# Optimization experiments

Hardware: AMD Instinct MI355X
Metric: run time of the kernel (lower is better)

## Reference

```python
import jax, jax.numpy as jnp
import numpy as np

B, T, D, E, H, F, K = 4, 2048, 2048, 16, 1024, 1024, 2


def setup_inputs() -> dict:
    key = jax.random.key(0)
    ks = jax.random.split(key, 7)
    sD, sH, sF = D ** -0.5, H ** -0.5, F ** -0.5
    hidden_state = jax.random.normal(ks[0], (B, T, D), jnp.float32)
    Wr = jax.random.normal(ks[1], (D, E), jnp.float32) * sD      # router
    Wg = jax.random.normal(ks[2], (D, 1), jnp.float32) * sD      # shared gate
    W1 = jax.random.normal(ks[3], (E, D, H), jnp.float32) * sD   # expert up-proj
    W2 = jax.random.normal(ks[4], (E, H, D), jnp.float32) * sH   # expert down-proj
    W1s = jax.random.normal(ks[5], (D, F), jnp.float32) * sD     # shared expert up
    W2s = jax.random.normal(ks[6], (F, D), jnp.float32) * sF     # shared expert down
    return {"hidden_state": hidden_state, "Wr": Wr, "Wg": Wg,
            "W1": W1, "W2": W2, "W1s": W1s, "W2s": W2s}


def reference(hidden_state, Wr, Wg, W1, W2, W1s, W2s):
    b, t, d = hidden_state.shape
    N = b * t
    x = hidden_state.reshape(N, d)

    # Router: softmax scores + shared-expert sigmoid gate
    s = jax.nn.softmax(x @ Wr, axis=-1)           # [N, E]
    g_shared = jax.nn.sigmoid(x @ Wg)             # [N, 1]

    topk_vals, topk_idx = jax.lax.top_k(s, K)     # [N, K]

    # Dense combine weights: gate[n,e] = topk_vals if expert e chosen, else 0.
    # Mathematically identical to sort/gather/scatter-add dispatch in the source.
    gate = jnp.zeros((N, E), dtype=s.dtype).at[
        jnp.arange(N)[:, None], topk_idx].add(topk_vals)

    # Per-expert FFN (fixed small expert loop), gate-weighted combine
    y = jnp.zeros_like(x)
    for e in range(E):
        h = jax.nn.gelu(x @ W1[e], approximate=False)   # [N, H]
        y = y + gate[:, e:e + 1] * (h @ W2[e])

    # Shared expert, scaled by sigmoid gate
    shared = jax.nn.gelu(x @ W1s, approximate=False) @ W2s
    y = y + g_shared * shared
    y_out = y.reshape(b, t, d)

    # Aux stats (attention_mask is None branch)
    importance = s.mean(axis=0)                               # [E]
    counts = jnp.zeros((E,), jnp.float32).at[topk_idx.reshape(-1)].add(1.0)
    load = counts / (counts.sum() + 1e-12)
    return y_out, importance, load
```

## Files before the change

### kernel.cpp

```cpp
#include <hip/hip_runtime.h>
#include <hip/hip_bf16.h>


#define N_TOK 8192
#define DDIM  2048
#define NEXP  16
#define HDIM  1024
#define FDIM  1024
#define NASSIGN (N_TOK * 2)

typedef __attribute__((ext_vector_type(8))) short bf16x8;
typedef __attribute__((ext_vector_type(4))) float f32x4;
typedef __attribute__((ext_vector_type(8))) unsigned short u16x8;
typedef __attribute__((ext_vector_type(4))) unsigned short u16x4;

__device__ inline unsigned short f2bf(float f) {
    unsigned int u = __builtin_bit_cast(unsigned int, f);
    u += 0x7FFFu + ((u >> 16) & 1u);
    return (unsigned short)(u >> 16);
}

__device__ inline float gelu_f(float v) {
    return 0.5f * v * (1.0f + erff(v * 0.7071067811865475f));
}

__device__ inline void gld16(void* lds, const void* g) {
    __builtin_amdgcn_global_load_lds(
        (const __attribute__((address_space(1))) unsigned int*)g,
        (__attribute__((address_space(3))) unsigned int*)lds, 16, 0, 0);
}

__global__ __launch_bounds__(256) void zero_small(float* imp) {
    if (threadIdx.x < NEXP) imp[threadIdx.x] = 0.0f;
}

__global__ __launch_bounds__(256) void cast_x_kernel(const float* __restrict__ x,
                                                     unsigned short* __restrict__ xb) {
    size_t i = (size_t)blockIdx.x * 256 + threadIdx.x;
    const float4 a = ((const float4*)x)[i * 2];
    const float4 b = ((const float4*)x)[i * 2 + 1];
    u16x8 o;
    o[0] = f2bf(a.x); o[1] = f2bf(a.y); o[2] = f2bf(a.z); o[3] = f2bf(a.w);
    o[4] = f2bf(b.x); o[5] = f2bf(b.y); o[6] = f2bf(b.z); o[7] = f2bf(b.w);
    *(u16x8*)(xb + i * 8) = o;
}

template <int R, int C>
__global__ __launch_bounds__(256) void transpose_cast(const float* __restrict__ src,
                                                      unsigned short* __restrict__ dst) {
    __shared__ unsigned short t[64][66];
    const size_t zoff = (size_t)blockIdx.z * R * C;
    src += zoff; dst += zoff;
    const int r0 = blockIdx.y * 64, c0 = blockIdx.x * 64;
    const int tid = threadIdx.x;
    const int cr = tid >> 4;
    const int cc4 = (tid & 15) * 4;
#pragma unroll
    for (int it = 0; it < 4; ++it) {
        int row = cr + it * 16;
        const float4 v = *(const float4*)(src + (size_t)(r0 + row) * C + c0 + cc4);
        t[row][cc4 + 0] = f2bf(v.x); t[row][cc4 + 1] = f2bf(v.y);
        t[row][cc4 + 2] = f2bf(v.z); t[row][cc4 + 3] = f2bf(v.w);
    }
    __syncthreads();
#pragma unroll
    for (int it = 0; it < 4; ++it) {
        int cc = cr + it * 16;
        u16x4 o;
#pragma unroll
        for (int j = 0; j < 4; ++j) o[j] = t[cc4 + j][cc];
        *(u16x4*)(dst + (size_t)(c0 + cc) * R + r0 + cc4) = o;
    }
}

__global__ __launch_bounds__(256) void router_kernel(
    const float* __restrict__ x, const float* __restrict__ Wr, const float* __restrict__ Wg,
    float* __restrict__ gsh, int* __restrict__ t2i, float* __restrict__ t2v,
    float* __restrict__ imp) {
    __shared__ float simp[NEXP];
    const int tid = threadIdx.x, lane = tid & 63, w = tid >> 6;
    if (tid < NEXP) simp[tid] = 0.0f;
    __syncthreads();
    const int n = blockIdx.x * 4 + w;
    const float* xr = x + (size_t)n * DDIM;
    float acc[NEXP];
#pragma unroll
    for (int e = 0; e < NEXP; ++e) acc[e] = 0.0f;
    float ag = 0.0f;
    for (int j = 0; j < DDIM / 64; ++j) {
        int d = lane + j * 64;
        float xv = xr[d];
        const float* wr = Wr + (size_t)d * NEXP;
#pragma unroll
        for (int e = 0; e < NEXP; ++e) acc[e] = fmaf(xv, wr[e], acc[e]);
        ag = fmaf(xv, Wg[d], ag);
    }
#pragma unroll
    for (int off = 32; off; off >>= 1) {
#pragma unroll
        for (int e = 0; e < NEXP; ++e) acc[e] += __shfl_xor(acc[e], off);
        ag += __shfl_xor(ag, off);
    }
    if (lane == 0) {
        float mx = acc[0];
#pragma unroll
        for (int e = 1; e < NEXP; ++e) mx = fmaxf(mx, acc[e]);
        float p[NEXP], s = 0.0f;
#pragma unroll
        for (int e = 0; e < NEXP; ++e) { p[e] = expf(acc[e] - mx); s += p[e]; }
        const float inv = 1.0f / s;
        int i1 = 0; float v1 = -1.0f;
#pragma unroll
        for (int e = 0; e < NEXP; ++e) {
            p[e] *= inv;
            if (p[e] > v1) { v1 = p[e]; i1 = e; }
        }
        int i2 = 0; float v2 = -1.0f;
#pragma unroll
        for (int e = 0; e < NEXP; ++e) {
            if (e != i1 && p[e] > v2) { v2 = p[e]; i2 = e; }
        }
        t2i[2 * n] = i1; t2i[2 * n + 1] = i2;
        t2v[2 * n] = v1; t2v[2 * n + 1] = v2;
        gsh[n] = 1.0f / (1.0f + expf(-ag));
#pragma unroll
        for (int e = 0; e < NEXP; ++e) atomicAdd(&simp[e], p[e]);
    }
    __syncthreads();
    if (tid < NEXP) unsafeAtomicAdd(&imp[tid], simp[tid]);
}

__global__ __launch_bounds__(256) void scan_finalize(
    const int* __restrict__ t2i, const float* __restrict__ imp,
    int* __restrict__ offs, int* __restrict__ fill, float* __restrict__ out_tail) {
    __shared__ int hist[NEXP];
    const int tid = threadIdx.x;
    if (tid < NEXP) hist[tid] = 0;
    __syncthreads();
    for (int i = tid; i < NASSIGN; i += 256) atomicAdd(&hist[t2i[i]], 1);
    __syncthreads();
    if (tid == 0) {
        int o = 0;
        for (int e = 0; e < NEXP; ++e) { offs[e] = o; o += hist[e]; }
        offs[NEXP] = o;
    }
    if (tid < NEXP) {
        fill[tid] = 0;
        out_tail[tid] = imp[tid] * (1.0f / (float)N_TOK);
        out_tail[NEXP + tid] = (float)hist[tid] / (float)NASSIGN;
    }
}

__global__ __launch_bounds__(256) void build_assign(
    const int* __restrict__ t2i, const float* __restrict__ t2v,
    const int* __restrict__ offs, int* __restrict__ fill,
    int* __restrict__ atok, float* __restrict__ agate) {
    const int n = blockIdx.x * 256 + threadIdx.x;
#pragma unroll
    for (int k = 0; k < 2; ++k) {
        int e = t2i[2 * n + k];
        int pos = offs[e] + atomicAdd(&fill[e], 1);
        atok[pos] = n;
        agate[pos] = t2v[2 * n + k];
    }
}

template <int MODE>
__global__ __launch_bounds__(256) void gemm_tile(
    const unsigned short* __restrict__ A, const unsigned short* __restrict__ B,
    float* __restrict__ Y, unsigned short* __restrict__ Hb,
    const int* __restrict__ offs, const int* __restrict__ atok,
    const float* __restrict__ agate, const float* __restrict__ gsh) {
    constexpr int KD = (MODE == 0 || MODE == 2) ? DDIM : HDIM;
    constexpr int NC = (MODE == 0 || MODE == 2) ? HDIM : DDIM;
    const int e = blockIdx.z;
    int m0 = 0, mE = N_TOK;
    if (MODE <= 1) { m0 = offs[e]; mE = offs[e + 1] - m0; }
    const int tm = blockIdx.y;
    if (tm * 128 >= mE) return;
    const int n0 = blockIdx.x * 128;

    __shared__ __align__(16) unsigned short As[128 * 32];
    __shared__ __align__(16) unsigned short Bs[128 * 32];

    const int tid = threadIdx.x, lane = tid & 63;
    const int wid = tid >> 6, wm = wid >> 1, wn = wid & 1;

    const unsigned short* srcA[2];
    const unsigned short* srcB[2];
    char* dstA[2];
    char* dstB[2];
#pragma unroll
    for (int it = 0; it < 2; ++it) {
        int c = tid + it * 256;
        int row = c >> 2, slot = c & 3;
        int ksw = (slot ^ ((row >> 1) & 3)) * 8;
        int arow = tm * 128 + row;
        if (MODE == 0) {
            int ar = arow < mE ? arow : mE - 1;
            srcA[it] = A + (size_t)atok[m0 + ar] * DDIM + ksw;
        } else if (MODE == 1) {
            int ar = arow < mE ? arow : mE - 1;
            srcA[it] = A + (size_t)(m0 + ar) * HDIM + ksw;
        } else {
            srcA[it] = A + (size_t)arow * KD + ksw;
        }
        srcB[it] = B + (MODE <= 1 ? (size_t)e * KD * NC : (size_t)0)
                     + (size_t)(n0 + row) * KD + ksw;
        dstA[it] = (char*)As + c * 16;
        dstB[it] = (char*)Bs + c * 16;
    }

    f32x4 acc[4][4] = {};

#pragma unroll 1
    for (int kk = 0; kk < KD; kk += 32) {
        if (kk) __syncthreads();
        gld16(dstA[0], srcA[0] + kk);
        gld16(dstA[1], srcA[1] + kk);
        gld16(dstB[0], srcB[0] + kk);
        gld16(dstB[1], srcB[1] + kk);
        __syncthreads();
        bf16x8 av[4], bv[4];
#pragma unroll
        for (int mi = 0; mi < 4; ++mi) {
            int r = wm * 64 + mi * 16 + (lane & 15);
            int s = (lane >> 4) ^ ((r >> 1) & 3);
            av[mi] = *(const bf16x8*)((const char*)As + r * 64 + s * 16);
        }
#pragma unroll
        for (int ni = 0; ni < 4; ++ni) {
            int r = wn * 64 + ni * 16 + (lane & 15);
            int s = (lane >> 4) ^ ((r >> 1) & 3);
            bv[ni] = *(const bf16x8*)((const char*)Bs + r * 64 + s * 16);
        }
#pragma unroll
        for (int mi = 0; mi < 4; ++mi)
#pragma unroll
            for (int ni = 0; ni < 4; ++ni)
                acc[mi][ni] = __builtin_amdgcn_mfma_f32_16x16x32_bf16(
                    av[mi], bv[ni], acc[mi][ni], 0, 0, 0);
    }

    const int col = lane & 15, r4 = (lane >> 4) * 4;
#pragma unroll
    for (int mi = 0; mi < 4; ++mi) {
#pragma unroll
        for (int r = 0; r < 4; ++r) {
            int grow = tm * 128 + wm * 64 + mi * 16 + r4 + r;
            if (MODE <= 1 && grow >= mE) continue;
            float gate = 1.0f; int tok = 0; float g3 = 0.0f;
            if (MODE == 0) gate = agate[m0 + grow];
            if (MODE == 1) tok = atok[m0 + grow];
            if (MODE == 3) g3 = gsh[grow];
#pragma unroll
            for (int ni = 0; ni < 4; ++ni) {
                int gcol = n0 + wn * 64 + ni * 16 + col;
                float v = acc[mi][ni][r];
                if (MODE == 0) {
                    Hb[(size_t)(m0 + grow) * HDIM + gcol] = f2bf(gelu_f(v) * gate);
                } else if (MODE == 1) {
                    unsafeAtomicAdd(&Y[(size_t)tok * DDIM + gcol], v);
                } else if (MODE == 2) {
                    Hb[(size_t)grow * HDIM + gcol] = f2bf(gelu_f(v));
                } else {
                    Y[(size_t)grow * DDIM + gcol] = g3 * v;
                }
            }
        }
    }
}

extern "C" void kernel_launch(void* const* d_in, const int* in_sizes, int n_in,
                              void* d_out, int out_size, void* d_ws, size_t ws_size,
                              hipStream_t stream) {
    const float* x   = (const float*)d_in[0];
    const float* Wr  = (const float*)d_in[1];
    const float* Wg  = (const float*)d_in[2];
    const float* W1  = (const float*)d_in[3];
    const float* W2  = (const float*)d_in[4];
    const float* W1s = (const float*)d_in[5];
    const float* W2s = (const float*)d_in[6];
    float* out = (float*)d_out;

    char* ws = (char*)d_ws;
    size_t off = 0;
    auto carve = [&](size_t bytes) { char* p = ws + off; off += (bytes + 255) & ~(size_t)255; return p; };
    unsigned short* xb    = (unsigned short*)carve((size_t)N_TOK * DDIM * 2);
    unsigned short* w1t   = (unsigned short*)carve((size_t)NEXP * DDIM * HDIM * 2);
    unsigned short* w2t   = (unsigned short*)carve((size_t)NEXP * HDIM * DDIM * 2);
    unsigned short* w1st  = (unsigned short*)carve((size_t)DDIM * FDIM * 2);
    unsigned short* w2st  = (unsigned short*)carve((size_t)FDIM * DDIM * 2);
    unsigned short* hb    = (unsigned short*)carve((size_t)NASSIGN * HDIM * 2);
    unsigned short* hs    = (unsigned short*)carve((size_t)N_TOK * FDIM * 2);
    float* gsh            = (float*)carve((size_t)N_TOK * 4);
    int* t2i              = (int*)carve((size_t)N_TOK * 2 * 4);
    float* t2v            = (float*)carve((size_t)N_TOK * 2 * 4);
    int* atok             = (int*)carve((size_t)NASSIGN * 4);
    float* agate          = (float*)carve((size_t)NASSIGN * 4);
    float* imp            = (float*)carve(256);
    int* offs             = (int*)carve(256);
    int* fill             = (int*)carve(256);
    if (ws_size < off) return;

    float* out_tail = out + (size_t)N_TOK * DDIM;

    hipLaunchKernelGGL(zero_small, dim3(1), dim3(256), 0, stream, imp);
    hipLaunchKernelGGL(cast_x_kernel, dim3(N_TOK * DDIM / 8 / 256), dim3(256), 0, stream, x, xb);
    hipLaunchKernelGGL((transpose_cast<DDIM, HDIM>), dim3(HDIM / 64, DDIM / 64, NEXP), dim3(256), 0, stream, W1, w1t);
    hipLaunchKernelGGL((transpose_cast<HDIM, DDIM>), dim3(DDIM / 64, HDIM / 64, NEXP), dim3(256), 0, stream, W2, w2t);
    hipLaunchKernelGGL((transpose_cast<DDIM, FDIM>), dim3(FDIM / 64, DDIM / 64, 1), dim3(256), 0, stream, W1s, w1st);
    hipLaunchKernelGGL((transpose_cast<FDIM, DDIM>), dim3(DDIM / 64, FDIM / 64, 1), dim3(256), 0, stream, W2s, w2st);
    hipLaunchKernelGGL(router_kernel, dim3(N_TOK / 4), dim3(256), 0, stream, x, Wr, Wg, gsh, t2i, t2v, imp);
    hipLaunchKernelGGL(scan_finalize, dim3(1), dim3(256), 0, stream, t2i, imp, offs, fill, out_tail);
    hipLaunchKernelGGL(build_assign, dim3(N_TOK / 256), dim3(256), 0, stream, t2i, t2v, offs, fill, atok, agate);

    hipLaunchKernelGGL((gemm_tile<2>), dim3(HDIM / 128, N_TOK / 128, 1), dim3(256), 0, stream,
                       xb, w1st, out, hs, offs, atok, agate, gsh);
    hipLaunchKernelGGL((gemm_tile<3>), dim3(DDIM / 128, N_TOK / 128, 1), dim3(256), 0, stream,
                       hs, w2st, out, nullptr, offs, atok, agate, gsh);
    hipLaunchKernelGGL((gemm_tile<0>), dim3(HDIM / 128, N_TOK / 128, NEXP), dim3(256), 0, stream,
                       xb, w1t, nullptr, hb, offs, atok, agate, gsh);
    hipLaunchKernelGGL((gemm_tile<1>), dim3(DDIM / 128, N_TOK / 128, NEXP), dim3(256), 0, stream,
                       hb, w2t, out, nullptr, offs, atok, agate, gsh);
}
```

Baseline: 685.2 us.

## Double-buffer GEMM LDS tiles and replace atomic scatter with bf16 combine pass

The GEMM main loop now uses two LDS buffers, so the next K-slice is prefetched while MFMAs run on the current one, with a single barrier per step. The expert down-projection no longer does fp32 atomic adds into the output. It writes per-assignment bf16 results into a reused workspace (the W1 transposed buffer, which is dead by then), and a new combine kernel gathers each token's two contributions through a position map. This removes atomic contention at the cost of an extra kernel, an extra read/write of the output, and bf16 rounding of the expert outputs.

```diff
diff --git a/kernel.cpp b/kernel.cpp
--- a/kernel.cpp
+++ b/kernel.cpp
@@ -18,6 +18,10 @@
     unsigned int u = __builtin_bit_cast(unsigned int, f);
     u += 0x7FFFu + ((u >> 16) & 1u);
     return (unsigned short)(u >> 16);
+}
+
+__device__ inline float bf2f(unsigned short h) {
+    return __builtin_bit_cast(float, (unsigned int)h << 16);
 }
 
 __device__ inline float gelu_f(float v) {
@@ -154,7 +158,7 @@
 __global__ __launch_bounds__(256) void build_assign(
     const int* __restrict__ t2i, const float* __restrict__ t2v,
     const int* __restrict__ offs, int* __restrict__ fill,
-    int* __restrict__ atok, float* __restrict__ agate) {
+    int* __restrict__ atok, float* __restrict__ agate, int* __restrict__ t2pos) {
     const int n = blockIdx.x * 256 + threadIdx.x;
 #pragma unroll
     for (int k = 0; k < 2; ++k) {
@@ -162,7 +166,32 @@
         int pos = offs[e] + atomicAdd(&fill[e], 1);
         atok[pos] = n;
         agate[pos] = t2v[2 * n + k];
-    }
+        t2pos[2 * n + k] = pos;
+    }
+}
+
+__global__ __launch_bounds__(256) void combine_kernel(
+    const unsigned short* __restrict__ contrib, const int* __restrict__ t2pos,
+    float* __restrict__ y) {
+    const int gi = blockIdx.x * 256 + threadIdx.x;
+    const int n = gi >> 8;
+    const int d8 = (gi & 255) * 8;
+    const int p0 = t2pos[2 * n], p1 = t2pos[2 * n + 1];
+    u16x8 a = *(const u16x8*)(contrib + (size_t)p0 * DDIM + d8);
+    u16x8 b = *(const u16x8*)(contrib + (size_t)p1 * DDIM + d8);
+    float* yr = y + (size_t)n * DDIM + d8;
+    float4 y0 = *(float4*)yr;
+    float4 y1 = *(float4*)(yr + 4);
+    y0.x += bf2f(a[0]) + bf2f(b[0]);
+    y0.y += bf2f(a[1]) + bf2f(b[1]);
+    y0.z += bf2f(a[2]) + bf2f(b[2]);
+    y0.w += bf2f(a[3]) + bf2f(b[3]);
+    y1.x += bf2f(a[4]) + bf2f(b[4]);
+    y1.y += bf2f(a[5]) + bf2f(b[5]);
+    y1.z += bf2f(a[6]) + bf2f(b[6]);
+    y1.w += bf2f(a[7]) + bf2f(b[7]);
+    *(float4*)yr = y0;
+    *(float4*)(yr + 4) = y1;
 }
 
 template <int MODE>
@@ -180,16 +209,15 @@
     if (tm * 128 >= mE) return;
     const int n0 = blockIdx.x * 128;
 
-    __shared__ __align__(16) unsigned short As[128 * 32];
-    __shared__ __align__(16) unsigned short Bs[128 * 32];
+    __shared__ __align__(16) unsigned short As[2][128 * 32];
+    __shared__ __align__(16) unsigned short Bs[2][128 * 32];
 
     const int tid = threadIdx.x, lane = tid & 63;
     const int wid = tid >> 6, wm = wid >> 1, wn = wid & 1;
 
-    const unsigned short* srcA[2];
-    const unsigned short* srcB[2];
-    char* dstA[2];
-    char* dstB[2];
+    const unsigned short* sA[2];
+    const unsigned short* sB[2];
+    int dOff[2];
 #pragma unroll
     for (int it = 0; it < 2; ++it) {
         int c = tid + it * 256;
@@ -198,41 +226,39 @@
         int arow = tm * 128 + row;
         if (MODE == 0) {
             int ar = arow < mE ? arow : mE - 1;
-            srcA[it] = A + (size_t)atok[m0 + ar] * DDIM + ksw;
+            sA[it] = A + (size_t)atok[m0 + ar] * DDIM + ksw;
         } else if (MODE == 1) {
             int ar = arow < mE ? arow : mE - 1;
-            srcA[it] = A + (size_t)(m0 + ar) * HDIM + ksw;
+            sA[it] = A + (size_t)(m0 + ar) * HDIM + ksw;
         } else {
-            srcA[it] = A + (size_t)arow * KD + ksw;
-        }
-        srcB[it] = B + (MODE <= 1 ? (size_t)e * KD * NC : (size_t)0)
-                     + (size_t)(n0 + row) * KD + ksw;
-        dstA[it] = (char*)As + c * 16;
-        dstB[it] = (char*)Bs + c * 16;
+            sA[it] = A + (size_t)arow * KD + ksw;
+        }
+        sB[it] = B + (MODE <= 1 ? (size_t)e * KD * NC : (size_t)0)
+                   + (size_t)(n0 + row) * KD + ksw;
+        dOff[it] = c * 16;
     }
 
     f32x4 acc[4][4] = {};
 
-#pragma unroll 1
-    for (int kk = 0; kk < KD; kk += 32) {
-        if (kk) __syncthreads();
-        gld16(dstA[0], srcA[0] + kk);
-        gld16(dstA[1], srcA[1] + kk);
-        gld16(dstB[0], srcB[0] + kk);
-        gld16(dstB[1], srcB[1] + kk);
-        __syncthreads();
+    auto stage = [&](int b, int kk) {
+        gld16((char*)As[b] + dOff[0], sA[0] + kk);
+        gld16((char*)As[b] + dOff[1], sA[1] + kk);
+        gld16((char*)Bs[b] + dOff[0], sB[0] + kk);
+        gld16((char*)Bs[b] + dOff[1], sB[1] + kk);
+    };
+    auto compute = [&](int b) {
         bf16x8 av[4], bv[4];
 #pragma unroll
         for (int mi = 0; mi < 4; ++mi) {
             int r = wm * 64 + mi * 16 + (lane & 15);
             int s = (lane >> 4) ^ ((r >> 1) & 3);
-            av[mi] = *(const bf16x8*)((const char*)As + r * 64 + s * 16);
+            av[mi] = *(const bf16x8*)((const char*)As[b] + r * 64 + s * 16);
         }
 #pragma unroll
         for (int ni = 0; ni < 4; ++ni) {
             int r = wn * 64 + ni * 16 + (lane & 15);
             int s = (lane >> 4) ^ ((r >> 1) & 3);
-            bv[ni] = *(const bf16x8*)((const char*)Bs + r * 64 + s * 16);
+            bv[ni] = *(const bf16x8*)((const char*)Bs[b] + r * 64 + s * 16);
         }
 #pragma unroll
         for (int mi = 0; mi < 4; ++mi)
@@ -240,6 +266,19 @@
             for (int ni = 0; ni < 4; ++ni)
                 acc[mi][ni] = __builtin_amdgcn_mfma_f32_16x16x32_bf16(
                     av[mi], bv[ni], acc[mi][ni], 0, 0, 0);
+    };
+
+    stage(0, 0);
+    __syncthreads();
+
+#pragma unroll 1
+    for (int kk = 0; kk < KD; kk += 64) {
+        stage(1, kk + 32);
+        compute(0);
+        __syncthreads();
+        if (kk + 64 < KD) stage(0, kk + 64);
+        compute(1);
+        __syncthreads();
     }
 
     const int col = lane & 15, r4 = (lane >> 4) * 4;
@@ -249,9 +288,8 @@
         for (int r = 0; r < 4; ++r) {
             int grow = tm * 128 + wm * 64 + mi * 16 + r4 + r;
             if (MODE <= 1 && grow >= mE) continue;
-            float gate = 1.0f; int tok = 0; float g3 = 0.0f;
+            float gate = 1.0f; float g3 = 0.0f;
             if (MODE == 0) gate = agate[m0 + grow];
-            if (MODE == 1) tok = atok[m0 + grow];
             if (MODE == 3) g3 = gsh[grow];
 #pragma unroll
             for (int ni = 0; ni < 4; ++ni) {
@@ -260,7 +298,7 @@
                 if (MODE == 0) {
                     Hb[(size_t)(m0 + grow) * HDIM + gcol] = f2bf(gelu_f(v) * gate);
                 } else if (MODE == 1) {
-                    unsafeAtomicAdd(&Y[(size_t)tok * DDIM + gcol], v);
+                    Hb[(size_t)(m0 + grow) * DDIM + gcol] = f2bf(v);
                 } else if (MODE == 2) {
                     Hb[(size_t)grow * HDIM + gcol] = f2bf(gelu_f(v));
                 } else {
@@ -298,10 +336,13 @@
     float* t2v            = (float*)carve((size_t)N_TOK * 2 * 4);
     int* atok             = (int*)carve((size_t)NASSIGN * 4);
     float* agate          = (float*)carve((size_t)NASSIGN * 4);
+    int* t2pos            = (int*)carve((size_t)NASSIGN * 4);
     float* imp            = (float*)carve(256);
     int* offs             = (int*)carve(256);
     int* fill             = (int*)carve(256);
     if (ws_size < off) return;
+
+    unsigned short* contrib = w1t;
 
     float* out_tail = out + (size_t)N_TOK * DDIM;
 
@@ -313,7 +354,7 @@
     hipLaunchKernelGGL((transpose_cast<FDIM, DDIM>), dim3(DDIM / 64, FDIM / 64, 1), dim3(256), 0, stream, W2s, w2st);
     hipLaunchKernelGGL(router_kernel, dim3(N_TOK / 4), dim3(256), 0, stream, x, Wr, Wg, gsh, t2i, t2v, imp);
     hipLaunchKernelGGL(scan_finalize, dim3(1), dim3(256), 0, stream, t2i, imp, offs, fill, out_tail);
-    hipLaunchKernelGGL(build_assign, dim3(N_TOK / 256), dim3(256), 0, stream, t2i, t2v, offs, fill, atok, agate);
+    hipLaunchKernelGGL(build_assign, dim3(N_TOK / 256), dim3(256), 0, stream, t2i, t2v, offs, fill, atok, agate, t2pos);
 
     hipLaunchKernelGGL((gemm_tile<2>), dim3(HDIM / 128, N_TOK / 128, 1), dim3(256), 0, stream,
                        xb, w1st, out, hs, offs, atok, agate, gsh);
@@ -322,5 +363,7 @@
     hipLaunchKernelGGL((gemm_tile<0>), dim3(HDIM / 128, N_TOK / 128, NEXP), dim3(256), 0, stream,
                        xb, w1t, nullptr, hb, offs, atok, agate, gsh);
     hipLaunchKernelGGL((gemm_tile<1>), dim3(DDIM / 128, N_TOK / 128, NEXP), dim3(256), 0, stream,
-                       hb, w2t, out, nullptr, offs, atok, agate, gsh);
-}
+                       hb, w2t, nullptr, contrib, offs, atok, agate, gsh);
+    hipLaunchKernelGGL(combine_kernel, dim3(N_TOK * DDIM / 8 / 256), dim3(256), 0, stream,
+                       contrib, t2pos, out);
+}
```

Measured after the change: 668.8 us. -2.4%, faster.

## Merge shared expert into grouped GEMM with 256x256 pipelined tiles and separate combine

Applied to the files above, without the earlier changes.

Treats the shared expert as a 17th expert so one pair of grouped GEMM launches covers all FFNs. The GEMM moves to 256x256 tiles with 512 threads, a 64-wide K step, double-buffered global-to-LDS loads interleaved with MFMA phases, and priority hints. The down-projection now writes bf16 per-assignment rows instead of issuing fp32 atomics, and a combine kernel sums the two expert rows plus the gated shared row per token. This removes atomic traffic and raises data reuse, at the cost of a bf16 intermediate, which adds rounding error and an extra memory pass. The contrib buffer aliases the start of the workspace, where xb and the W1 copy live.

```diff
diff --git a/kernel.cpp b/kernel.cpp
--- a/kernel.cpp
+++ b/kernel.cpp
@@ -8,6 +8,7 @@
 #define HDIM  1024
 #define FDIM  1024
 #define NASSIGN (N_TOK * 2)
+#define NROWS (NASSIGN + N_TOK)
 
 typedef __attribute__((ext_vector_type(8))) short bf16x8;
 typedef __attribute__((ext_vector_type(4))) float f32x4;
@@ -18,6 +19,10 @@
     unsigned int u = __builtin_bit_cast(unsigned int, f);
     u += 0x7FFFu + ((u >> 16) & 1u);
     return (unsigned short)(u >> 16);
+}
+
+__device__ inline float bf2f(unsigned short h) {
+    return __builtin_bit_cast(float, (unsigned int)h << 16);
 }
 
 __device__ inline float gelu_f(float v) {
@@ -143,6 +148,7 @@
         int o = 0;
         for (int e = 0; e < NEXP; ++e) { offs[e] = o; o += hist[e]; }
         offs[NEXP] = o;
+        offs[NEXP + 1] = NROWS;
     }
     if (tid < NEXP) {
         fill[tid] = 0;
@@ -154,7 +160,7 @@
 __global__ __launch_bounds__(256) void build_assign(
     const int* __restrict__ t2i, const float* __restrict__ t2v,
     const int* __restrict__ offs, int* __restrict__ fill,
-    int* __restrict__ atok, float* __restrict__ agate) {
+    int* __restrict__ atok, float* __restrict__ agate, int* __restrict__ t2pos) {
     const int n = blockIdx.x * 256 + threadIdx.x;
 #pragma unroll
     for (int k = 0; k < 2; ++k) {
@@ -162,110 +168,183 @@
         int pos = offs[e] + atomicAdd(&fill[e], 1);
         atok[pos] = n;
         agate[pos] = t2v[2 * n + k];
-    }
-}
+        t2pos[2 * n + k] = pos;
+    }
+    atok[NASSIGN + n] = n;
+    agate[NASSIGN + n] = 1.0f;
+}
+
+__global__ __launch_bounds__(256) void combine_kernel(
+    const unsigned short* __restrict__ contrib, const int* __restrict__ t2pos,
+    const float* __restrict__ gsh, float* __restrict__ y) {
+    const int gi = blockIdx.x * 256 + threadIdx.x;
+    const int n = gi >> 8;
+    const int d8 = (gi & 255) * 8;
+    const int p0 = t2pos[2 * n], p1 = t2pos[2 * n + 1];
+    const float g = gsh[n];
+    u16x8 a = *(const u16x8*)(contrib + (size_t)p0 * DDIM + d8);
+    u16x8 b = *(const u16x8*)(contrib + (size_t)p1 * DDIM + d8);
+    u16x8 c = *(const u16x8*)(contrib + (size_t)(NASSIGN + n) * DDIM + d8);
+    float4 y0, y1;
+    y0.x = bf2f(a[0]) + bf2f(b[0]) + g * bf2f(c[0]);
+    y0.y = bf2f(a[1]) + bf2f(b[1]) + g * bf2f(c[1]);
+    y0.z = bf2f(a[2]) + bf2f(b[2]) + g * bf2f(c[2]);
+    y0.w = bf2f(a[3]) + bf2f(b[3]) + g * bf2f(c[3]);
+    y1.x = bf2f(a[4]) + bf2f(b[4]) + g * bf2f(c[4]);
+    y1.y = bf2f(a[5]) + bf2f(b[5]) + g * bf2f(c[5]);
+    y1.z = bf2f(a[6]) + bf2f(b[6]) + g * bf2f(c[6]);
+    y1.w = bf2f(a[7]) + bf2f(b[7]) + g * bf2f(c[7]);
+    float* yr = y + (size_t)n * DDIM + d8;
+    *(float4*)yr = y0;
+    *(float4*)(yr + 4) = y1;
+}
+
+#define BAR()   __builtin_amdgcn_s_barrier()
+#define WAITL() do { asm volatile("s_waitcnt lgkmcnt(0)" ::: "memory"); \
+                     __builtin_amdgcn_sched_barrier(0); } while (0)
+
+#define RD_A(dst, mb) do {                                                  \
+  _Pragma("unroll") for (int i_ = 0; i_ < 4; ++i_)                          \
+  _Pragma("unroll") for (int kh_ = 0; kh_ < 2; ++kh_)                       \
+    (dst)[i_][kh_] = *(const bf16x8*)(aB + rbA[kh_] + ((mb) + i_) * 2048);  \
+} while (0)
+
+#define RD_B(dst, nb) do {                                                  \
+  _Pragma("unroll") for (int i_ = 0; i_ < 2; ++i_)                          \
+  _Pragma("unroll") for (int kh_ = 0; kh_ < 2; ++kh_)                       \
+    (dst)[i_][kh_] = *(const bf16x8*)(bB + rbB[kh_] + ((nb) + i_) * 2048);  \
+} while (0)
+
+#define MM(mb, nb, a_, b_) do {                                             \
+  __builtin_amdgcn_s_setprio(1);                                            \
+  _Pragma("unroll") for (int i_ = 0; i_ < 4; ++i_)                          \
+  _Pragma("unroll") for (int n_ = 0; n_ < 2; ++n_)                          \
+  _Pragma("unroll") for (int kh_ = 0; kh_ < 2; ++kh_)                       \
+    acc[(mb) + i_][(nb) + n_] = __builtin_amdgcn_mfma_f32_16x16x32_bf16(    \
+        (a_)[i_][kh_], (b_)[n_][kh_], acc[(mb) + i_][(nb) + n_], 0, 0, 0);  \
+  __builtin_amdgcn_s_setprio(0);                                            \
+} while (0)
+
+#define STG(dstbuf, src, kt) do {                                           \
+    gld16((char*)(dstbuf) + ldso0, (src)[0] + (size_t)(kt) * 64);           \
+    gld16((char*)(dstbuf) + ldso1, (src)[1] + (size_t)(kt) * 64);           \
+} while (0)
+
+#define KTILE(d, t) do {                                                    \
+    const char* aB = (const char*)As_[d][wm];                               \
+    const char* bB = (const char*)Bs_[d][bh];                               \
+    const int ka = ((t) + 1 < NT) ? (t) + 1 : (t);                          \
+    const int kb = ((t) + 2 < NT) ? (t) + 2 : (t);                          \
+    bf16x8 av[4][2], bv0[2][2], bv1[2][2];                                  \
+    RD_A(av, 0); RD_B(bv0, 0);                                              \
+    STG(As_[(d) ^ 1][0], sA[0], ka);                                        \
+    BAR(); WAITL();                                                         \
+    MM(0, 0, av, bv0);                                                      \
+    BAR();                                                                  \
+    RD_B(bv1, 2);                                                           \
+    STG(As_[(d) ^ 1][1], sA[1], ka);                                        \
+    BAR(); WAITL();                                                         \
+    MM(0, 2, av, bv1);                                                      \
+    BAR();                                                                  \
+    RD_A(av, 4);                                                            \
+    STG(Bs_[d][0], sB[0], kb);                                              \
+    BAR(); WAITL();                                                         \
+    MM(4, 0, av, bv0);                                                      \
+    BAR();                                                                  \
+    STG(Bs_[d][1], sB[1], kb);                                              \
+    BAR();                                                                  \
+    MM(4, 2, av, bv1);                                                      \
+    asm volatile("s_waitcnt vmcnt(4)" ::: "memory");                        \
+    BAR();                                                                  \
+} while (0)
 
 template <int MODE>
-__global__ __launch_bounds__(256) void gemm_tile(
+__global__ __launch_bounds__(512, 2) void gemm8(
     const unsigned short* __restrict__ A, const unsigned short* __restrict__ B,
-    float* __restrict__ Y, unsigned short* __restrict__ Hb,
+    unsigned short* __restrict__ out,
     const int* __restrict__ offs, const int* __restrict__ atok,
-    const float* __restrict__ agate, const float* __restrict__ gsh) {
-    constexpr int KD = (MODE == 0 || MODE == 2) ? DDIM : HDIM;
-    constexpr int NC = (MODE == 0 || MODE == 2) ? HDIM : DDIM;
+    const float* __restrict__ agate) {
+    constexpr int KD = MODE == 0 ? DDIM : HDIM;
+    constexpr int NC = MODE == 0 ? HDIM : DDIM;
+    constexpr int NT = KD / 64;
     const int e = blockIdx.z;
-    int m0 = 0, mE = N_TOK;
-    if (MODE <= 1) { m0 = offs[e]; mE = offs[e + 1] - m0; }
+    const int m0 = offs[e];
+    const int mE = offs[e + 1] - m0;
     const int tm = blockIdx.y;
-    if (tm * 128 >= mE) return;
-    const int n0 = blockIdx.x * 128;
-
-    __shared__ __align__(16) unsigned short As[128 * 32];
-    __shared__ __align__(16) unsigned short Bs[128 * 32];
-
-    const int tid = threadIdx.x, lane = tid & 63;
-    const int wid = tid >> 6, wm = wid >> 1, wn = wid & 1;
-
-    const unsigned short* srcA[2];
-    const unsigned short* srcB[2];
-    char* dstA[2];
-    char* dstB[2];
-#pragma unroll
-    for (int it = 0; it < 2; ++it) {
-        int c = tid + it * 256;
-        int row = c >> 2, slot = c & 3;
-        int ksw = (slot ^ ((row >> 1) & 3)) * 8;
-        int arow = tm * 128 + row;
-        if (MODE == 0) {
-            int ar = arow < mE ? arow : mE - 1;
-            srcA[it] = A + (size_t)atok[m0 + ar] * DDIM + ksw;
-        } else if (MODE == 1) {
-            int ar = arow < mE ? arow : mE - 1;
-            srcA[it] = A + (size_t)(m0 + ar) * HDIM + ksw;
-        } else {
-            srcA[it] = A + (size_t)arow * KD + ksw;
+    if (tm * 256 >= mE) return;
+    const int n0 = blockIdx.x * 256;
+
+    __shared__ __align__(16) unsigned short As_[2][2][128 * 64];
+    __shared__ __align__(16) unsigned short Bs_[2][2][128 * 64];
+
+    const int tid = threadIdx.x;
+    const int lane = tid & 63, w = tid >> 6;
+    const int wm = w >> 2, wn = w & 3;
+    const int bh = wn >> 1;
+
+    const int kch = ((lane & 7) ^ ((lane >> 3) & 7)) * 8;
+    const int ldso0 = (w * 128 + lane) * 16;
+    const int ldso1 = (w * 128 + 64 + lane) * 16;
+    const unsigned short* sA[2][2];
+    const unsigned short* sB[2][2];
+#pragma unroll
+    for (int h = 0; h < 2; ++h) {
+#pragma unroll
+        for (int j = 0; j < 2; ++j) {
+            int rr = h * 128 + w * 16 + j * 8 + (lane >> 3);
+            int ar = tm * 256 + rr; ar = ar < mE ? ar : mE - 1;
+            if (MODE == 0)
+                sA[h][j] = A + (size_t)atok[m0 + ar] * KD + kch;
+            else
+                sA[h][j] = A + (size_t)(m0 + ar) * KD + kch;
+            sB[h][j] = B + (size_t)e * KD * NC + (size_t)(n0 + rr) * KD + kch;
         }
-        srcB[it] = B + (MODE <= 1 ? (size_t)e * KD * NC : (size_t)0)
-                     + (size_t)(n0 + row) * KD + ksw;
-        dstA[it] = (char*)As + c * 16;
-        dstB[it] = (char*)Bs + c * 16;
-    }
-
-    f32x4 acc[4][4] = {};
+    }
+
+    const int c16 = lane & 15, q = lane >> 4;
+    int rbA[2], rbB[2];
+#pragma unroll
+    for (int kh = 0; kh < 2; ++kh) {
+        int sl = (kh * 4 + q) ^ (c16 & 7);
+        rbA[kh] = c16 * 128 + sl * 16;
+        rbB[kh] = ((wn & 1) * 64 + c16) * 128 + sl * 16;
+    }
+
+    f32x4 acc[8][4];
+#pragma unroll
+    for (int i = 0; i < 8; ++i)
+#pragma unroll
+        for (int j = 0; j < 4; ++j) acc[i][j] = (f32x4){0.f, 0.f, 0.f, 0.f};
+
+    STG(As_[0][0], sA[0], 0); STG(As_[0][1], sA[1], 0);
+    STG(Bs_[0][0], sB[0], 0); STG(Bs_[0][1], sB[1], 0);
+    STG(Bs_[1][0], sB[0], 1); STG(Bs_[1][1], sB[1], 1);
+    asm volatile("s_waitcnt vmcnt(4)" ::: "memory");
+    BAR();
 
 #pragma unroll 1
-    for (int kk = 0; kk < KD; kk += 32) {
-        if (kk) __syncthreads();
-        gld16(dstA[0], srcA[0] + kk);
-        gld16(dstA[1], srcA[1] + kk);
-        gld16(dstB[0], srcB[0] + kk);
-        gld16(dstB[1], srcB[1] + kk);
-        __syncthreads();
-        bf16x8 av[4], bv[4];
-#pragma unroll
-        for (int mi = 0; mi < 4; ++mi) {
-            int r = wm * 64 + mi * 16 + (lane & 15);
-            int s = (lane >> 4) ^ ((r >> 1) & 3);
-            av[mi] = *(const bf16x8*)((const char*)As + r * 64 + s * 16);
-        }
-#pragma unroll
-        for (int ni = 0; ni < 4; ++ni) {
-            int r = wn * 64 + ni * 16 + (lane & 15);
-            int s = (lane >> 4) ^ ((r >> 1) & 3);
-            bv[ni] = *(const bf16x8*)((const char*)Bs + r * 64 + s * 16);
-        }
-#pragma unroll
-        for (int mi = 0; mi < 4; ++mi)
-#pragma unroll
-            for (int ni = 0; ni < 4; ++ni)
-                acc[mi][ni] = __builtin_amdgcn_mfma_f32_16x16x32_bf16(
-                    av[mi], bv[ni], acc[mi][ni], 0, 0, 0);
+    for (int it = 0; it < NT / 2; ++it) {
+        const int t0 = it * 2;
+        KTILE(0, t0);
+        KTILE(1, t0 + 1);
     }
 
     const int col = lane & 15, r4 = (lane >> 4) * 4;
 #pragma unroll
-    for (int mi = 0; mi < 4; ++mi) {
+    for (int mi = 0; mi < 8; ++mi) {
 #pragma unroll
         for (int r = 0; r < 4; ++r) {
-            int grow = tm * 128 + wm * 64 + mi * 16 + r4 + r;
-            if (MODE <= 1 && grow >= mE) continue;
-            float gate = 1.0f; int tok = 0; float g3 = 0.0f;
-            if (MODE == 0) gate = agate[m0 + grow];
-            if (MODE == 1) tok = atok[m0 + grow];
-            if (MODE == 3) g3 = gsh[grow];
+            int grow = tm * 256 + wm * 128 + mi * 16 + r4 + r;
+            if (grow >= mE) continue;
+            float gate = (MODE == 0) ? agate[m0 + grow] : 0.0f;
 #pragma unroll
             for (int ni = 0; ni < 4; ++ni) {
                 int gcol = n0 + wn * 64 + ni * 16 + col;
                 float v = acc[mi][ni][r];
-                if (MODE == 0) {
-                    Hb[(size_t)(m0 + grow) * HDIM + gcol] = f2bf(gelu_f(v) * gate);
-                } else if (MODE == 1) {
-                    unsafeAtomicAdd(&Y[(size_t)tok * DDIM + gcol], v);
-                } else if (MODE == 2) {
-                    Hb[(size_t)grow * HDIM + gcol] = f2bf(gelu_f(v));
-                } else {
-                    Y[(size_t)grow * DDIM + gcol] = g3 * v;
-                }
+                if (MODE == 0)
+                    out[(size_t)(m0 + grow) * NC + gcol] = f2bf(gelu_f(v) * gate);
+                else
+                    out[(size_t)(m0 + grow) * NC + gcol] = f2bf(v);
             }
         }
     }
@@ -287,40 +366,40 @@
     size_t off = 0;
     auto carve = [&](size_t bytes) { char* p = ws + off; off += (bytes + 255) & ~(size_t)255; return p; };
     unsigned short* xb    = (unsigned short*)carve((size_t)N_TOK * DDIM * 2);
-    unsigned short* w1t   = (unsigned short*)carve((size_t)NEXP * DDIM * HDIM * 2);
-    unsigned short* w2t   = (unsigned short*)carve((size_t)NEXP * HDIM * DDIM * 2);
-    unsigned short* w1st  = (unsigned short*)carve((size_t)DDIM * FDIM * 2);
-    unsigned short* w2st  = (unsigned short*)carve((size_t)FDIM * DDIM * 2);
-    unsigned short* hb    = (unsigned short*)carve((size_t)NASSIGN * HDIM * 2);
-    unsigned short* hs    = (unsigned short*)carve((size_t)N_TOK * FDIM * 2);
+    unsigned short* w1all = (unsigned short*)carve((size_t)(NEXP + 1) * DDIM * HDIM * 2);
+    unsigned short* w2all = (unsigned short*)carve((size_t)(NEXP + 1) * HDIM * DDIM * 2);
+    unsigned short* hb    = (unsigned short*)carve((size_t)NROWS * HDIM * 2);
     float* gsh            = (float*)carve((size_t)N_TOK * 4);
     int* t2i              = (int*)carve((size_t)N_TOK * 2 * 4);
     float* t2v            = (float*)carve((size_t)N_TOK * 2 * 4);
-    int* atok             = (int*)carve((size_t)NASSIGN * 4);
-    float* agate          = (float*)carve((size_t)NASSIGN * 4);
+    int* atok             = (int*)carve((size_t)NROWS * 4);
+    float* agate          = (float*)carve((size_t)NROWS * 4);
+    int* t2pos            = (int*)carve((size_t)NASSIGN * 4);
     float* imp            = (float*)carve(256);
     int* offs             = (int*)carve(256);
     int* fill             = (int*)carve(256);
     if (ws_size < off) return;
 
+    unsigned short* contrib = (unsigned short*)ws;
+
     float* out_tail = out + (size_t)N_TOK * DDIM;
 
     hipLaunchKernelGGL(zero_small, dim3(1), dim3(256), 0, stream, imp);
     hipLaunchKernelGGL(cast_x_kernel, dim3(N_TOK * DDIM / 8 / 256), dim3(256), 0, stream, x, xb);
-    hipLaunchKernelGGL((transpose_cast<DDIM, HDIM>), dim3(HDIM / 64, DDIM / 64, NEXP), dim3(256), 0, stream, W1, w1t);
-    hipLaunchKernelGGL((transpose_cast<HDIM, DDIM>), dim3(DDIM / 64, HDIM / 64, NEXP), dim3(256), 0, stream, W2, w2t);
-    hipLaunchKernelGGL((transpose_cast<DDIM, FDIM>), dim3(FDIM / 64, DDIM / 64, 1), dim3(256), 0, stream, W1s, w1st);
-    hipLaunchKernelGGL((transpose_cast<FDIM, DDIM>), dim3(DDIM / 64, FDIM / 64, 1), dim3(256), 0, stream, W2s, w2st);
+    hipLaunchKernelGGL((transpose_cast<DDIM, HDIM>), dim3(HDIM / 64, DDIM / 64, NEXP), dim3(256), 0, stream, W1, w1all);
+    hipLaunchKernelGGL((transpose_cast<DDIM, HDIM>), dim3(HDIM / 64, DDIM / 64, 1), dim3(256), 0, stream,
+                       W1s, w1all + (size_t)NEXP * DDIM * HDIM);
+    hipLaunchKernelGGL((transpose_cast<HDIM, DDIM>), dim3(DDIM / 64, HDIM / 64, NEXP), dim3(256), 0, stream, W2, w2all);
+    hipLaunchKernelGGL((transpose_cast<HDIM, DDIM>), dim3(DDIM / 64, HDIM / 64, 1), dim3(256), 0, stream,
+                       W2s, w2all + (size_t)NEXP * HDIM * DDIM);
     hipLaunchKernelGGL(router_kernel, dim3(N_TOK / 4), dim3(256), 0, stream, x, Wr, Wg, gsh, t2i, t2v, imp);
     hipLaunchKernelGGL(scan_finalize, dim3(1), dim3(256), 0, stream, t2i, imp, offs, fill, out_tail);
-    hipLaunchKernelGGL(build_assign, dim3(N_TOK / 256), dim3(256), 0, stream, t2i, t2v, offs, fill, atok, agate);
-
-    hipLaunchKernelGGL((gemm_tile<2>), dim3(HDIM / 128, N_TOK / 128, 1), dim3(256), 0, stream,
-                       xb, w1st, out, hs, offs, atok, agate, gsh);
-    hipLaunchKernelGGL((gemm_tile<3>), dim3(DDIM / 128, N_TOK / 128, 1), dim3(256), 0, stream,
-                       hs, w2st, out, nullptr, offs, atok, agate, gsh);
-    hipLaunchKernelGGL((gemm_tile<0>), dim3(HDIM / 128, N_TOK / 128, NEXP), dim3(256), 0, stream,
-                       xb, w1t, nullptr, hb, offs, atok, agate, gsh);
-    hipLaunchKernelGGL((gemm_tile<1>), dim3(DDIM / 128, N_TOK / 128, NEXP), dim3(256), 0, stream,
-                       hb, w2t, out, nullptr, offs, atok, agate, gsh);
-}
+    hipLaunchKernelGGL(build_assign, dim3(N_TOK / 256), dim3(256), 0, stream, t2i, t2v, offs, fill, atok, agate, t2pos);
+
+    hipLaunchKernelGGL((gemm8<0>), dim3(HDIM / 256, N_TOK / 256, NEXP + 1), dim3(512), 0, stream,
+                       xb, w1all, hb, offs, atok, agate);
+    hipLaunchKernelGGL((gemm8<1>), dim3(DDIM / 256, N_TOK / 256, NEXP + 1), dim3(512), 0, stream,
+                       hb, w2all, contrib, offs, atok, agate);
+    hipLaunchKernelGGL(combine_kernel, dim3(N_TOK * DDIM / 8 / 256), dim3(256), 0, stream,
+                       contrib, t2pos, gsh, out);
+}
```

Measured after the change: 724.3 us. 5.7% more time.
